# Kernel optimization log

Hardware: AMD Instinct MI355X
Metric: run time of the kernel (lower is better)

## Reference

```python
import jax, jax.numpy as jnp
import numpy as np

N = 50000
E = 800000
IN_C, HID_C, OUT_C = 128, 256, 128
BN_EPS = 1e-5


def glorot(key, shape):
    fan_in, fan_out = shape
    lim = float(np.sqrt(6.0 / (fan_in + fan_out)))
    return jax.random.uniform(key, shape, jnp.float32, -lim, lim)


def setup_inputs() -> dict:
    key = jax.random.key(0)
    ks = jax.random.split(key, 16)
    inp = {
        "x": jax.random.normal(ks[0], (N, IN_C), jnp.float32),
        "edge_index": jax.random.randint(ks[1], (2, E), 0, N, jnp.int64),
        # SAGEConv 1 (in->hid): lin_l has bias, lin_r has no bias (PyG default)
        "wl1": glorot(ks[2], (IN_C, HID_C)), "bl1": jnp.zeros((HID_C,), jnp.float32),
        "wr1": glorot(ks[3], (IN_C, HID_C)),
        # SAGEConv 2 (hid->hid)
        "wl2": glorot(ks[4], (HID_C, HID_C)), "bl2": jnp.zeros((HID_C,), jnp.float32),
        "wr2": glorot(ks[5], (HID_C, HID_C)),
        # SAGEConv 3 (hid->out)
        "wl3": glorot(ks[6], (HID_C, OUT_C)), "bl3": jnp.zeros((OUT_C,), jnp.float32),
        "wr3": glorot(ks[7], (HID_C, OUT_C)),
        # BatchNorm params (eval mode: running stats)
        "bn1_w": jnp.ones((HID_C,), jnp.float32), "bn1_b": jnp.zeros((HID_C,), jnp.float32),
        "bn1_m": jax.random.normal(ks[8], (HID_C,), jnp.float32) * 0.1,
        "bn1_v": jax.random.uniform(ks[9], (HID_C,), jnp.float32, 0.5, 1.5),
        "bn2_w": jnp.ones((HID_C,), jnp.float32), "bn2_b": jnp.zeros((HID_C,), jnp.float32),
        "bn2_m": jax.random.normal(ks[10], (HID_C,), jnp.float32) * 0.1,
        "bn2_v": jax.random.uniform(ks[11], (HID_C,), jnp.float32, 0.5, 1.5),
    }
    return inp


def sage_conv(x, src, dst, wl, bl, wr):
    # mean aggregation of source-node features at destination nodes
    agg = jax.ops.segment_sum(x[src], dst, num_segments=N)          # [N, d_in]
    deg = jax.ops.segment_sum(jnp.ones((E,), x.dtype), dst, num_segments=N)
    mean = agg / jnp.maximum(deg, 1.0)[:, None]
    return mean @ wl + bl + x @ wr                                   # [N, d_out]


def batch_norm(x, w, b, m, v):
    return (x - m) * jax.lax.rsqrt(v + BN_EPS) * w + b


def reference(x, edge_index, wl1, bl1, wr1, wl2, bl2, wr2, wl3, bl3, wr3,
              bn1_w, bn1_b, bn1_m, bn1_v, bn2_w, bn2_b, bn2_m, bn2_v):
    src, dst = edge_index[0], edge_index[1]
    # layer 1: SAGEConv -> BN -> ReLU (dropout is identity in eval mode)
    h = sage_conv(x, src, dst, wl1, bl1, wr1)
    h = jax.nn.relu(batch_norm(h, bn1_w, bn1_b, bn1_m, bn1_v))
    # layer 2
    h = sage_conv(h, src, dst, wl2, bl2, wr2)
    h = jax.nn.relu(batch_norm(h, bn2_w, bn2_b, bn2_m, bn2_v))
    # output layer: plain SAGEConv
    return sage_conv(h, src, dst, wl3, bl3, wr3)
```

## Files before the change

kernel.cpp:

```cpp
#include <hip/hip_runtime.h>
#include <hip/hip_bf16.h>

#define NN 50000
#define NE 800000
#define NSB 49
#define AGG_BLOCKS 2048

typedef __attribute__((ext_vector_type(8))) short bh8;
typedef __attribute__((ext_vector_type(4))) float f32x4;

static __device__ __forceinline__ unsigned short f2bf(float f){
  unsigned u = __float_as_uint(f);
  unsigned r = (u + 0x7fffu + ((u >> 16) & 1u)) >> 16;
  return (unsigned short)r;
}
static __device__ __forceinline__ float bflo(unsigned u){ return __uint_as_float(u << 16); }
static __device__ __forceinline__ float bfhi(unsigned u){ return __uint_as_float(u & 0xffff0000u); }
static __device__ __forceinline__ unsigned packbf2(float lo, float hi){
  return ((unsigned)f2bf(hi) << 16) | (unsigned)f2bf(lo);
}

static __device__ __forceinline__ void gload16(const void* g, void* l){
  __builtin_amdgcn_global_load_lds(
      (const __attribute__((address_space(1))) unsigned int*)g,
      (__attribute__((address_space(3))) unsigned int*)l, 16, 0, 0);
}

__global__ void hist_k(const int* __restrict__ dstv, int* __restrict__ cnt,
                       int* __restrict__ rank){
  int i = blockIdx.x * 256 + threadIdx.x;
  if (i < NE) rank[i] = atomicAdd(&cnt[dstv[i]], 1);
}

__global__ __launch_bounds__(256) void scan1_k(const int* __restrict__ cnt,
                                               int* __restrict__ rowp,
                                               int* __restrict__ bsum){
  __shared__ int sa[256], sb[256];
  const int t = threadIdx.x, blk = blockIdx.x;
  const int base = blk * 1024 + t * 4;
  int4 v = make_int4(0, 0, 0, 0);
  if (base + 3 < NN) v = *reinterpret_cast<const int4*>(cnt + base);
  else if (base < NN){
    v.x = cnt[base];
    if (base + 1 < NN) v.y = cnt[base + 1];
    if (base + 2 < NN) v.z = cnt[base + 2];
  }
  const int s = v.x + v.y + v.z + v.w;
  sa[t] = s; __syncthreads();
  int* a = sa; int* b = sb;
  for (int off = 1; off < 256; off <<= 1){
    int val = a[t]; if (t >= off) val += a[t - off];
    b[t] = val; __syncthreads();
    int* tmp = a; a = b; b = tmp;
  }
  const int ex = a[t] - s;
  if (base < NN){
    rowp[base] = ex;
    if (base + 1 < NN) rowp[base + 1] = ex + v.x;
    if (base + 2 < NN) rowp[base + 2] = ex + v.x + v.y;
    if (base + 3 < NN) rowp[base + 3] = ex + v.x + v.y + v.z;
  }
  if (t == 255) bsum[blk] = a[255];
}

__global__ void scan2_k(int* __restrict__ bsum){
  __shared__ int s[64];
  const int t = threadIdx.x;
  s[t] = (t < NSB) ? bsum[t] : 0;
  __syncthreads();
  if (t == 0){
    int run = 0;
    for (int i = 0; i < NSB; ++i){ int c = s[i]; s[i] = run; run += c; }
  }
  __syncthreads();
  if (t < NSB) bsum[t] = s[t];
}

__global__ __launch_bounds__(256) void scan3_k(int* __restrict__ rowp,
                                               const int* __restrict__ bsum){
  const int blk = blockIdx.x;
  const int base = blk * 1024 + threadIdx.x * 4;
  const int off = bsum[blk];
  #pragma unroll
  for (int i = 0; i < 4; ++i){
    int idx = base + i;
    if (idx < NN) rowp[idx] += off;
  }
  if (blk == 0 && threadIdx.x == 0) rowp[NN] = NE;
}

__global__ __launch_bounds__(256) void fill_k(const int* __restrict__ srcv,
                       const int* __restrict__ dstv,
                       const int* __restrict__ rank,
                       const int* __restrict__ rowp, int* __restrict__ csrc){
  const int part  = blockIdx.x & 7;
  const int chunk = blockIdx.x >> 3;
  const int lo = part * (NN / 8);
  const int hi = lo + (NN / 8);
  const int base = chunk * (NE / 128);
  const int endi = base + (NE / 128);
  for (int i = base + threadIdx.x; i < endi; i += 256){
    int d = dstv[i];
    if (d >= lo && d < hi){
      csrc[rowp[d] + rank[i]] = srcv[i];
    }
  }
}

__global__ void f2b_k(const float4* __restrict__ x, uint2* __restrict__ xb){
  int i = blockIdx.x * 256 + threadIdx.x;
  if (i < NN * 128 / 4){
    float4 v = x[i];
    uint2 o; o.x = packbf2(v.x, v.y); o.y = packbf2(v.z, v.w);
    xb[i] = o;
  }
}

__global__ void f8conv_k(const uint4* __restrict__ h1, uint2* __restrict__ h1q){
  int i = blockIdx.x * 256 + threadIdx.x;
  if (i < NN * 256 / 8){
    uint4 v = h1[i];
    float f0 = bflo(v.x), f1 = bfhi(v.x), f2 = bflo(v.y), f3 = bfhi(v.y);
    float f4 = bflo(v.z), f5 = bfhi(v.z), f6 = bflo(v.w), f7 = bfhi(v.w);
    int w0 = 0, w1 = 0;
    w0 = __builtin_amdgcn_cvt_pk_fp8_f32(f0, f1, w0, false);
    w0 = __builtin_amdgcn_cvt_pk_fp8_f32(f2, f3, w0, true);
    w1 = __builtin_amdgcn_cvt_pk_fp8_f32(f4, f5, w1, false);
    w1 = __builtin_amdgcn_cvt_pk_fp8_f32(f6, f7, w1, true);
    uint2 o; o.x = (unsigned)w0; o.y = (unsigned)w1;
    h1q[i] = o;
  }
}

__global__ void prep_k(const float* __restrict__ wl1, const float* __restrict__ wr1,
                       const float* __restrict__ wl2, const float* __restrict__ wr2,
                       const float* __restrict__ wl3, const float* __restrict__ wr3,
                       const float* __restrict__ bl1, const float* __restrict__ bl2,
                       const float* __restrict__ bn1w, const float* __restrict__ bn1b,
                       const float* __restrict__ bn1m, const float* __restrict__ bn1v,
                       const float* __restrict__ bn2w, const float* __restrict__ bn2b,
                       const float* __restrict__ bn2m, const float* __restrict__ bn2v,
                       unsigned short* __restrict__ B1t, unsigned short* __restrict__ B2t,
                       unsigned short* __restrict__ B3t,
                       float* __restrict__ S1, float* __restrict__ T1,
                       float* __restrict__ S2, float* __restrict__ T2){
  int i = blockIdx.x * 256 + threadIdx.x;
  if (i < 65536){
    int n = i >> 8, k = i & 255;
    float v = (k < 128) ? wl1[k * 256 + n] : wr1[(k - 128) * 256 + n];
    B1t[n * 256 + k] = f2bf(v);
  } else if (i < 65536 + 131072){
    int j = i - 65536; int n = j >> 9, k = j & 511;
    float v = (k < 256) ? wl2[k * 256 + n] : wr2[(k - 256) * 256 + n];
    B2t[n * 512 + k] = f2bf(v);
  } else if (i < 65536 + 131072 + 65536){
    int j = i - (65536 + 131072); int n = j >> 8, k = j & 255;
    float v = (n < 128) ? wl3[k * 128 + n] : wr3[k * 128 + (n - 128)];
    B3t[n * 256 + k] = f2bf(v);
  } else if (i < 65536 + 131072 + 65536 + 512){
    int j = i - (65536 + 131072 + 65536);
    if (j < 256){
      float s = bn1w[j] * rsqrtf(bn1v[j] + 1e-5f);
      S1[j] = s; T1[j] = (bl1[j] - bn1m[j]) * s + bn1b[j];
    } else {
      int c = j - 256;
      float s = bn2w[c] * rsqrtf(bn2v[c] + 1e-5f);
      S2[c] = s; T2[c] = (bl2[c] - bn2m[c]) * s + bn2b[c];
    }
  }
}

__global__ __launch_bounds__(256) void agg128_k(const unsigned* __restrict__ feat, unsigned* __restrict__ out,
                         const int* __restrict__ rowp, const int* __restrict__ csrc){
  const int lane = threadIdx.x & 63;
  const int node0 = __builtin_amdgcn_readfirstlane(blockIdx.x * 4 + (threadIdx.x >> 6));
  const int nw = gridDim.x * 4;
  for (int node = node0; node < NN; node += nw){
    const int start = rowp[node], end = rowp[node + 1];
    float a0 = 0.f, a1 = 0.f, b0 = 0.f, b1 = 0.f;
    int e = start;
    for (; e + 7 < end; e += 8){
      unsigned u0 = feat[(size_t)csrc[e]     * 64 + lane];
      unsigned u1 = feat[(size_t)csrc[e + 1] * 64 + lane];
      unsigned u2 = feat[(size_t)csrc[e + 2] * 64 + lane];
      unsigned u3 = feat[(size_t)csrc[e + 3] * 64 + lane];
      unsigned u4 = feat[(size_t)csrc[e + 4] * 64 + lane];
      unsigned u5 = feat[(size_t)csrc[e + 5] * 64 + lane];
      unsigned u6 = feat[(size_t)csrc[e + 6] * 64 + lane];
      unsigned u7 = feat[(size_t)csrc[e + 7] * 64 + lane];
      a0 += bflo(u0); a1 += bfhi(u0);
      b0 += bflo(u1); b1 += bfhi(u1);
      a0 += bflo(u2); a1 += bfhi(u2);
      b0 += bflo(u3); b1 += bfhi(u3);
      a0 += bflo(u4); a1 += bfhi(u4);
      b0 += bflo(u5); b1 += bfhi(u5);
      a0 += bflo(u6); a1 += bfhi(u6);
      b0 += bflo(u7); b1 += bfhi(u7);
    }
    for (; e < end; ++e){
      unsigned u = feat[(size_t)csrc[e] * 64 + lane];
      a0 += bflo(u); a1 += bfhi(u);
    }
    int d = end - start;
    float inv = 1.f / (float)(d > 0 ? d : 1);
    out[(size_t)node * 64 + lane] = packbf2((a0 + b0) * inv, (a1 + b1) * inv);
  }
}

#define DEC8(u, x0, x1, x2, x3) { \
  x0 += __builtin_amdgcn_cvt_f32_fp8((u), 0); \
  x1 += __builtin_amdgcn_cvt_f32_fp8((u), 1); \
  x2 += __builtin_amdgcn_cvt_f32_fp8((u), 2); \
  x3 += __builtin_amdgcn_cvt_f32_fp8((u), 3); }

__global__ __launch_bounds__(256) void agg256q_k(const unsigned* __restrict__ featq, unsigned* __restrict__ out,
                         const int* __restrict__ rowp, const int* __restrict__ csrc){
  const int lane = threadIdx.x & 63;
  const int node0 = __builtin_amdgcn_readfirstlane(blockIdx.x * 4 + (threadIdx.x >> 6));
  const int nw = gridDim.x * 4;
  for (int node = node0; node < NN; node += nw){
    const int start = rowp[node], end = rowp[node + 1];
    float a0 = 0.f, a1 = 0.f, a2 = 0.f, a3 = 0.f;
    float b0 = 0.f, b1 = 0.f, b2 = 0.f, b3 = 0.f;
    int e = start;
    for (; e + 7 < end; e += 8){
      unsigned u0 = featq[(size_t)csrc[e]     * 64 + lane];
      unsigned u1 = featq[(size_t)csrc[e + 1] * 64 + lane];
      unsigned u2 = featq[(size_t)csrc[e + 2] * 64 + lane];
      unsigned u3 = featq[(size_t)csrc[e + 3] * 64 + lane];
      unsigned u4 = featq[(size_t)csrc[e + 4] * 64 + lane];
      unsigned u5 = featq[(size_t)csrc[e + 5] * 64 + lane];
      unsigned u6 = featq[(size_t)csrc[e + 6] * 64 + lane];
      unsigned u7 = featq[(size_t)csrc[e + 7] * 64 + lane];
      DEC8(u0, a0, a1, a2, a3) DEC8(u1, b0, b1, b2, b3)
      DEC8(u2, a0, a1, a2, a3) DEC8(u3, b0, b1, b2, b3)
      DEC8(u4, a0, a1, a2, a3) DEC8(u5, b0, b1, b2, b3)
      DEC8(u6, a0, a1, a2, a3) DEC8(u7, b0, b1, b2, b3)
    }
    for (; e < end; ++e){
      unsigned u = featq[(size_t)csrc[e] * 64 + lane];
      DEC8(u, a0, a1, a2, a3)
    }
    int d = end - start;
    float inv = 1.f / (float)(d > 0 ? d : 1);
    uint2 o; o.x = packbf2((a0 + b0) * inv, (a1 + b1) * inv);
    o.y = packbf2((a2 + b2) * inv, (a3 + b3) * inv);
    *reinterpret_cast<uint2*>(out + (size_t)node * 128 + lane * 2) = o;
  }
}

__global__ __launch_bounds__(256) void final_k(const unsigned* __restrict__ t, float* __restrict__ out,
                        const int* __restrict__ rowp, const int* __restrict__ csrc,
                        const float* __restrict__ bl3){
  const int lane = threadIdx.x & 63;
  const int node0 = __builtin_amdgcn_readfirstlane(blockIdx.x * 4 + (threadIdx.x >> 6));
  const int nw = gridDim.x * 4;
  for (int node = node0; node < NN; node += nw){
    const int start = rowp[node], end = rowp[node + 1];
    float a0 = 0.f, a1 = 0.f, b0 = 0.f, b1 = 0.f;
    int e = start;
    for (; e + 7 < end; e += 8){
      unsigned u0 = t[(size_t)csrc[e]     * 64 + lane];
      unsigned u1 = t[(size_t)csrc[e + 1] * 64 + lane];
      unsigned u2 = t[(size_t)csrc[e + 2] * 64 + lane];
      unsigned u3 = t[(size_t)csrc[e + 3] * 64 + lane];
      unsigned u4 = t[(size_t)csrc[e + 4] * 64 + lane];
      unsigned u5 = t[(size_t)csrc[e + 5] * 64 + lane];
      unsigned u6 = t[(size_t)csrc[e + 6] * 64 + lane];
      unsigned u7 = t[(size_t)csrc[e + 7] * 64 + lane];
      a0 += bflo(u0); a1 += bfhi(u0);
      b0 += bflo(u1); b1 += bfhi(u1);
      a0 += bflo(u2); a1 += bfhi(u2);
      b0 += bflo(u3); b1 += bfhi(u3);
      a0 += bflo(u4); a1 += bfhi(u4);
      b0 += bflo(u5); b1 += bfhi(u5);
      a0 += bflo(u6); a1 += bfhi(u6);
      b0 += bflo(u7); b1 += bfhi(u7);
    }
    for (; e < end; ++e){
      unsigned u = t[(size_t)csrc[e] * 64 + lane];
      a0 += bflo(u); a1 += bfhi(u);
    }
    int d = end - start;
    float inv = 1.f / (float)(d > 0 ? d : 1);
    float2* o = reinterpret_cast<float2*>(out + (size_t)node * 128) + lane;
    float2 v = *o;
    v.x += (a0 + b0) * inv + bl3[lane * 2];
    v.y += (a1 + b1) * inv + bl3[lane * 2 + 1];
    *o = v;
  }
}

template<int KTOT, int K0, int MODE>
__global__ __launch_bounds__(256) void gemm_k(
    const unsigned short* __restrict__ A0, const unsigned short* __restrict__ A1,
    const unsigned short* __restrict__ Bt,
    const float* __restrict__ S, const float* __restrict__ Tt,
    unsigned short* __restrict__ outB, unsigned short* __restrict__ outT,
    float* __restrict__ outF, int M)
{
  __shared__ __align__(16) unsigned char lds[32768];
  const int tid = threadIdx.x;
  const int lane = tid & 63;
  const int wv = tid >> 6;
  const int wm = wv >> 1, wn = wv & 1;

  const int nwg = gridDim.x;
  const int q = nwg >> 3, r8 = nwg & 7;
  const int xcd = blockIdx.x & 7, idx = blockIdx.x >> 3;
  const int wg = (xcd < r8) ? xcd * (q + 1) + idx : r8 * (q + 1) + (xcd - r8) * q + idx;
  const int bm = wg >> 1, bn = wg & 1;

  const int rr0 = tid >> 2,         g0 = (tid & 3) ^ ((tid >> 3) & 3);
  const int rr1 = (tid + 256) >> 2, g1 = ((tid + 256) & 3) ^ (((tid + 256) >> 3) & 3);
  int growA0 = bm * 128 + rr0; if (growA0 > M - 1) growA0 = M - 1;
  int growA1 = bm * 128 + rr1; if (growA1 > M - 1) growA1 = M - 1;
  const size_t browA0 = (size_t)(bn * 128 + rr0) * KTOT;
  const size_t browA1 = (size_t)(bn * 128 + rr1) * KTOT;

  const int l15 = lane & 15, kg = lane >> 4;
  const int slot = (kg ^ ((l15 >> 1) & 3)) * 16;

  constexpr int NT = KTOT / 32;

  auto STAGE = [&](int buf, int kt){
    const int kb = kt * 32;
    const unsigned short* Ap; int pitch, kk;
    if (KTOT == K0 || kb < K0){ Ap = A0; pitch = K0; kk = kb; }
    else { Ap = A1; pitch = KTOT - K0; kk = kb - K0; }
    unsigned char* base = lds + buf * 16384;
    gload16(Ap + (size_t)growA0 * pitch + kk + g0 * 8, base + tid * 16);
    gload16(Ap + (size_t)growA1 * pitch + kk + g1 * 8, base + 4096 + tid * 16);
    gload16(Bt + browA0 + kb + g0 * 8, base + 8192 + tid * 16);
    gload16(Bt + browA1 + kb + g1 * 8, base + 12288 + tid * 16);
  };

  f32x4 acc[4][4];
  #pragma unroll
  for (int i = 0; i < 4; ++i)
    #pragma unroll
    for (int j = 0; j < 4; ++j){ acc[i][j][0]=0.f; acc[i][j][1]=0.f; acc[i][j][2]=0.f; acc[i][j][3]=0.f; }

  STAGE(0, 0);
  __syncthreads();

  for (int kt = 0; kt < NT; ++kt){
    if (kt + 1 < NT) STAGE((kt + 1) & 1, kt + 1);
    unsigned char* base = lds + (kt & 1) * 16384;

    bh8 af[4], bf[4];
    #pragma unroll
    for (int mi = 0; mi < 4; ++mi){
      int rA = wm * 64 + mi * 16 + l15;
      af[mi] = *reinterpret_cast<const bh8*>(base + rA * 64 + slot);
    }
    #pragma unroll
    for (int ni = 0; ni < 4; ++ni){
      int rB = wn * 64 + ni * 16 + l15;
      bf[ni] = *reinterpret_cast<const bh8*>(base + 8192 + rB * 64 + slot);
    }
    #pragma unroll
    for (int mi = 0; mi < 4; ++mi)
      #pragma unroll
      for (int ni = 0; ni < 4; ++ni)
        acc[mi][ni] = __builtin_amdgcn_mfma_f32_16x16x32_bf16(af[mi], bf[ni], acc[mi][ni], 0, 0, 0);
    __syncthreads();
  }

  #pragma unroll
  for (int mi = 0; mi < 4; ++mi){
    int rbase = bm * 128 + wm * 64 + mi * 16 + ((lane >> 4) << 2);
    #pragma unroll
    for (int ni = 0; ni < 4; ++ni){
      int col = bn * 128 + wn * 64 + ni * 16 + (lane & 15);
      #pragma unroll
      for (int j = 0; j < 4; ++j){
        int row = rbase + j;
        if (row < M){
          float v = acc[mi][ni][j];
          if (MODE == 0){
            v = v * S[col] + Tt[col];
            v = v > 0.f ? v : 0.f;
            outB[(size_t)row * 256 + col] = f2bf(v);
          } else {
            if (col < 128) outT[(size_t)row * 128 + col] = f2bf(v);
            else           outF[(size_t)row * 128 + (col - 128)] = v;
          }
        }
      }
    }
  }
}

extern "C" void kernel_launch(void* const* d_in, const int* in_sizes, int n_in,
                              void* d_out, int out_size, void* d_ws, size_t ws_size,
                              hipStream_t stream) {
  (void)in_sizes; (void)n_in; (void)out_size; (void)ws_size;
  const float* x   = (const float*)d_in[0];
  const int*   ei  = (const int*)d_in[1];
  const int*   srcv = ei;
  const int*   dstv = ei + NE;
  const float* wl1 = (const float*)d_in[2];
  const float* bl1 = (const float*)d_in[3];
  const float* wr1 = (const float*)d_in[4];
  const float* wl2 = (const float*)d_in[5];
  const float* bl2 = (const float*)d_in[6];
  const float* wr2 = (const float*)d_in[7];
  const float* wl3 = (const float*)d_in[8];
  const float* bl3 = (const float*)d_in[9];
  const float* wr3 = (const float*)d_in[10];
  const float* bn1w = (const float*)d_in[11];
  const float* bn1b = (const float*)d_in[12];
  const float* bn1m = (const float*)d_in[13];
  const float* bn1v = (const float*)d_in[14];
  const float* bn2w = (const float*)d_in[15];
  const float* bn2b = (const float*)d_in[16];
  const float* bn2m = (const float*)d_in[17];
  const float* bn2v = (const float*)d_in[18];

  char* ws = (char*)d_ws;
  size_t off = 0;
  auto alloc = [&](size_t bytes) -> void* {
    void* p = ws + off;
    off += (bytes + 255) & ~(size_t)255;
    return p;
  };
  int* cnt  = (int*)alloc((size_t)NN * 4);
  int* rank = (int*)alloc((size_t)NE * 4);
  int* rowp = (int*)alloc((size_t)(NN + 1) * 4);
  int* csrc = (int*)alloc((size_t)NE * 4);
  int* bsum = (int*)alloc((size_t)NSB * 4);
  unsigned short* B1t = (unsigned short*)alloc(256 * 256 * 2);
  unsigned short* B2t = (unsigned short*)alloc(256 * 512 * 2);
  unsigned short* B3t = (unsigned short*)alloc(256 * 256 * 2);
  float* S1 = (float*)alloc(256 * 4);
  float* T1 = (float*)alloc(256 * 4);
  float* S2 = (float*)alloc(256 * 4);
  float* T2 = (float*)alloc(256 * 4);
  unsigned short* xb   = (unsigned short*)alloc((size_t)NN * 128 * 2);
  unsigned short* agg1 = (unsigned short*)alloc((size_t)NN * 128 * 2);
  unsigned short* h1   = (unsigned short*)alloc((size_t)NN * 256 * 2);
  unsigned short* h2   = (unsigned short*)alloc((size_t)NN * 256 * 2);
  unsigned short* agg2 = xb;
  unsigned char*  h1q  = (unsigned char*)h2;
  unsigned short* tbuf = h1;
  float* outp = (float*)d_out;

  hipMemsetAsync(cnt, 0, (size_t)NN * 4, stream);
  hist_k<<<(NE + 255) / 256, 256, 0, stream>>>(dstv, cnt, rank);
  scan1_k<<<NSB, 256, 0, stream>>>(cnt, rowp, bsum);
  scan2_k<<<1, 64, 0, stream>>>(bsum);
  scan3_k<<<NSB, 256, 0, stream>>>(rowp, bsum);
  fill_k<<<1024, 256, 0, stream>>>(srcv, dstv, rank, rowp, csrc);
  prep_k<<<1026, 256, 0, stream>>>(wl1, wr1, wl2, wr2, wl3, wr3, bl1, bl2,
                                   bn1w, bn1b, bn1m, bn1v, bn2w, bn2b, bn2m, bn2v,
                                   B1t, B2t, B3t, S1, T1, S2, T2);
  f2b_k<<<(NN * 128 / 4 + 255) / 256, 256, 0, stream>>>((const float4*)x, (uint2*)xb);

  agg128_k<<<AGG_BLOCKS, 256, 0, stream>>>((const unsigned*)xb, (unsigned*)agg1, rowp, csrc);
  gemm_k<256, 128, 0><<<782, 256, 0, stream>>>(agg1, xb, B1t, S1, T1, h1, nullptr, nullptr, NN);
  f8conv_k<<<(NN * 256 / 8 + 255) / 256, 256, 0, stream>>>((const uint4*)h1, (uint2*)h1q);
  agg256q_k<<<AGG_BLOCKS, 256, 0, stream>>>((const unsigned*)h1q, (unsigned*)agg2, rowp, csrc);
  gemm_k<512, 256, 0><<<782, 256, 0, stream>>>(agg2, h1, B2t, S2, T2, h2, nullptr, nullptr, NN);
  gemm_k<256, 256, 1><<<782, 256, 0, stream>>>(h2, h2, B3t, nullptr, nullptr, nullptr, tbuf, outp, NN);
  final_k<<<AGG_BLOCKS, 256, 0, stream>>>((const unsigned*)tbuf, outp, rowp, csrc, bl3);
}
```

Baseline: 272.8 us.

## Load GEMM MFMA fragments directly from global into registers, dropping LDS staging

The GEMM kernel no longer stages A and B tiles through double-buffered LDS with barriers. Each wave now loads its MFMA operand fragments straight from global memory into registers and double-buffers them across k-steps. s_setprio is raised around the MFMA blocks. This removes LDS traffic and the block-wide syncs, but each wave re-reads data that other waves share, so L2/global load traffic goes up and the 16-byte per-lane loads are less coalesced.

New measurement: 345.3 us. +26.6%, slower.

```diff
diff --git a/kernel.cpp b/kernel.cpp
--- a/kernel.cpp
+++ b/kernel.cpp
@@ -18,12 +18,6 @@
 static __device__ __forceinline__ float bfhi(unsigned u){ return __uint_as_float(u & 0xffff0000u); }
 static __device__ __forceinline__ unsigned packbf2(float lo, float hi){
   return ((unsigned)f2bf(hi) << 16) | (unsigned)f2bf(lo);
-}
-
-static __device__ __forceinline__ void gload16(const void* g, void* l){
-  __builtin_amdgcn_global_load_lds(
-      (const __attribute__((address_space(1))) unsigned int*)g,
-      (__attribute__((address_space(3))) unsigned int*)l, 16, 0, 0);
 }
 
 __global__ void hist_k(const int* __restrict__ dstv, int* __restrict__ cnt,
@@ -299,7 +293,6 @@
     unsigned short* __restrict__ outB, unsigned short* __restrict__ outT,
     float* __restrict__ outF, int M)
 {
-  __shared__ __align__(16) unsigned char lds[32768];
   const int tid = threadIdx.x;
   const int lane = tid & 63;
   const int wv = tid >> 6;
@@ -311,28 +304,30 @@
   const int wg = (xcd < r8) ? xcd * (q + 1) + idx : r8 * (q + 1) + (xcd - r8) * q + idx;
   const int bm = wg >> 1, bn = wg & 1;
 
-  const int rr0 = tid >> 2,         g0 = (tid & 3) ^ ((tid >> 3) & 3);
-  const int rr1 = (tid + 256) >> 2, g1 = ((tid + 256) & 3) ^ (((tid + 256) >> 3) & 3);
-  int growA0 = bm * 128 + rr0; if (growA0 > M - 1) growA0 = M - 1;
-  int growA1 = bm * 128 + rr1; if (growA1 > M - 1) growA1 = M - 1;
-  const size_t browA0 = (size_t)(bn * 128 + rr0) * KTOT;
-  const size_t browA1 = (size_t)(bn * 128 + rr1) * KTOT;
-
   const int l15 = lane & 15, kg = lane >> 4;
-  const int slot = (kg ^ ((l15 >> 1) & 3)) * 16;
+
+  int arow[4];
+  #pragma unroll
+  for (int mi = 0; mi < 4; ++mi){
+    int r = bm * 128 + wm * 64 + mi * 16 + l15;
+    arow[mi] = (r > M - 1) ? (M - 1) : r;
+  }
 
   constexpr int NT = KTOT / 32;
 
-  auto STAGE = [&](int buf, int kt){
+  auto LOAD = [&](int kt, bh8 (&af)[4], bh8 (&bf)[4]){
     const int kb = kt * 32;
     const unsigned short* Ap; int pitch, kk;
     if (KTOT == K0 || kb < K0){ Ap = A0; pitch = K0; kk = kb; }
     else { Ap = A1; pitch = KTOT - K0; kk = kb - K0; }
-    unsigned char* base = lds + buf * 16384;
-    gload16(Ap + (size_t)growA0 * pitch + kk + g0 * 8, base + tid * 16);
-    gload16(Ap + (size_t)growA1 * pitch + kk + g1 * 8, base + 4096 + tid * 16);
-    gload16(Bt + browA0 + kb + g0 * 8, base + 8192 + tid * 16);
-    gload16(Bt + browA1 + kb + g1 * 8, base + 12288 + tid * 16);
+    #pragma unroll
+    for (int mi = 0; mi < 4; ++mi)
+      af[mi] = *reinterpret_cast<const bh8*>(Ap + (size_t)arow[mi] * pitch + kk + kg * 8);
+    #pragma unroll
+    for (int ni = 0; ni < 4; ++ni){
+      int n = bn * 128 + wn * 64 + ni * 16 + l15;
+      bf[ni] = *reinterpret_cast<const bh8*>(Bt + (size_t)n * KTOT + kb + kg * 8);
+    }
   };
 
   f32x4 acc[4][4];
@@ -341,30 +336,26 @@
     #pragma unroll
     for (int j = 0; j < 4; ++j){ acc[i][j][0]=0.f; acc[i][j][1]=0.f; acc[i][j][2]=0.f; acc[i][j][3]=0.f; }
 
-  STAGE(0, 0);
-  __syncthreads();
-
-  for (int kt = 0; kt < NT; ++kt){
-    if (kt + 1 < NT) STAGE((kt + 1) & 1, kt + 1);
-    unsigned char* base = lds + (kt & 1) * 16384;
-
-    bh8 af[4], bf[4];
-    #pragma unroll
-    for (int mi = 0; mi < 4; ++mi){
-      int rA = wm * 64 + mi * 16 + l15;
-      af[mi] = *reinterpret_cast<const bh8*>(base + rA * 64 + slot);
-    }
-    #pragma unroll
-    for (int ni = 0; ni < 4; ++ni){
-      int rB = wn * 64 + ni * 16 + l15;
-      bf[ni] = *reinterpret_cast<const bh8*>(base + 8192 + rB * 64 + slot);
-    }
+  bh8 afA[4], bfA[4], afB[4], bfB[4];
+  LOAD(0, afA, bfA);
+  #pragma unroll
+  for (int kt2 = 0; kt2 < NT; kt2 += 2){
+    if (kt2 + 1 < NT) LOAD(kt2 + 1, afB, bfB);
+    __builtin_amdgcn_s_setprio(1);
     #pragma unroll
     for (int mi = 0; mi < 4; ++mi)
       #pragma unroll
       for (int ni = 0; ni < 4; ++ni)
-        acc[mi][ni] = __builtin_amdgcn_mfma_f32_16x16x32_bf16(af[mi], bf[ni], acc[mi][ni], 0, 0, 0);
-    __syncthreads();
+        acc[mi][ni] = __builtin_amdgcn_mfma_f32_16x16x32_bf16(afA[mi], bfA[ni], acc[mi][ni], 0, 0, 0);
+    __builtin_amdgcn_s_setprio(0);
+    if (kt2 + 2 < NT) LOAD(kt2 + 2, afA, bfA);
+    __builtin_amdgcn_s_setprio(1);
+    #pragma unroll
+    for (int mi = 0; mi < 4; ++mi)
+      #pragma unroll
+      for (int ni = 0; ni < 4; ++ni)
+        acc[mi][ni] = __builtin_amdgcn_mfma_f32_16x16x32_bf16(afB[mi], bfB[ni], acc[mi][ni], 0, 0, 0);
+    __builtin_amdgcn_s_setprio(0);
   }
 
   #pragma unroll
```
